# Kernel tuning notes

Hardware: AMD Instinct MI355X
Metric: run time of the kernel (lower is better)

## Reference

```python
import jax, jax.numpy as jnp
import numpy as np

EMB = 1024
HEAD = 64


def setup_inputs() -> dict:
    key = jax.random.key(0)
    kx, kq, kk, kv = jax.random.split(key, 4)
    x = jax.random.normal(kx, (4, 4096, EMB), dtype=jnp.float32)
    # nn.Linear(emb, head, bias=False): y = x @ W^T; store transposed [emb, head]
    s = 1.0 / np.sqrt(EMB)
    Wq = jax.random.uniform(kq, (EMB, HEAD), jnp.float32, -s, s)
    Wk = jax.random.uniform(kk, (EMB, HEAD), jnp.float32, -s, s)
    Wv = jax.random.uniform(kv, (EMB, HEAD), jnp.float32, -s, s)
    return {"x": x, "Wq": Wq, "Wk": Wk, "Wv": Wv}


def reference(x, Wq, Wk, Wv):
    # x: [B, T, E]; projections -> [B, T, H]
    Q = jnp.einsum("bte,eh->bth", x, Wq)
    K = jnp.einsum("bte,eh->bth", x, Wk)
    V = jnp.einsum("bte,eh->bth", x, Wv)
    scale = 1.0 / np.sqrt(HEAD).astype(np.float32)
    scores = jnp.einsum("bqh,bkh->bqk", Q, K) * scale  # [B, T, T]
    attn = jax.nn.softmax(scores, axis=-1)
    out = jnp.einsum("bqk,bkh->bqh", attn, V)  # [B, T, H]
    return out
```

## Files before the change

### kernel.cpp

```cpp
#include <hip/hip_runtime.h>
#include <hip/hip_bf16.h>

typedef __bf16 bf16x8 __attribute__((ext_vector_type(8)));
typedef float floatx4 __attribute__((ext_vector_type(4)));

#define B_ 4
#define T_ 4096
#define E_ 1024
#define H_ 64
#define NSEG 8
#define SEGLEN (T_ / NSEG)
#define NROWS (B_ * T_)

#define QSCALE 0.18033688011112042f

#if __has_builtin(__builtin_amdgcn_exp2f)
#define EXP2(x) __builtin_amdgcn_exp2f(x)
#else
#define EXP2(x) exp2f(x)
#endif

__device__ __forceinline__ floatx4 mfma16(bf16x8 a, bf16x8 b, floatx4 c) {
  return __builtin_amdgcn_mfma_f32_16x16x32_bf16(a, b, c, 0, 0, 0);
}

#define GLDS16(gp, lp)                                                        \
  __builtin_amdgcn_global_load_lds(                                           \
      (const __attribute__((address_space(1))) void*)(gp),                    \
      (__attribute__((address_space(3))) void*)(lp), 16, 0, 0)

__global__ void prep_wt_k(const float* __restrict__ Wq, const float* __restrict__ Wk,
                          const float* __restrict__ Wv, __bf16* __restrict__ Wfrag) {
  int gid = blockIdx.x * 4 + (threadIdx.x >> 6);
  int lane = threadIdx.x & 63;
  int ch = gid / 24, rem = gid % 24;
  int nt = rem >> 1, half = rem & 1;
  int g = lane >> 4, lm = lane & 15;
  int w = nt >> 2;
  const float* W = (w == 0) ? Wq : (w == 1) ? Wk : Wv;
  float sc = (w == 0) ? QSCALE : 1.0f;
  int h = (nt & 3) * 16 + lm;
  int e0 = ch * 64 + half * 32 + g * 8;
  __bf16* dst = Wfrag + (size_t)gid * 1024 / 2 + lane * 8;
  bf16x8 v;
#pragma unroll
  for (int j = 0; j < 8; j++) v[j] = (__bf16)(W[(size_t)(e0 + j) * H_ + h] * sc);
  *(bf16x8*)dst = v;
}

__global__ void proj_k(const float* __restrict__ x, const __bf16* __restrict__ Wfrag,
                       __bf16* __restrict__ Qo, __bf16* __restrict__ Ko,
                       __bf16* __restrict__ Vt) {
  __shared__ __align__(16) char sX[2 * 4096];

  int tid = threadIdx.x;
  int wv = tid >> 6, lane = tid & 63;
  int lm = lane & 15, g = lane >> 4;
  int row_base = blockIdx.x * 16;

  floatx4 acc[3];
#pragma unroll
  for (int i = 0; i < 3; i++) acc[i] = (floatx4)0.0f;

  const char* xb = (const char*)x;
  const char* wfb = (const char*)Wfrag;
  int srow = tid >> 4, sc = tid & 15;

#define PROJ_STAGE(buf, ec)                                                   \
  GLDS16(xb + (size_t)(row_base + srow) * 4096 + (size_t)(ec) * 4 +           \
             ((sc ^ srow) << 4),                                              \
         sX + (buf) * 4096 + tid * 16);

  PROJ_STAGE(0, 0);
  __syncthreads();

  for (int ch = 0; ch < 16; ch++) {
    if (ch + 1 < 16) PROJ_STAGE((ch + 1) & 1, (ch + 1) * 64);
    const char* xB = sX + (ch & 1) * 4096;

    bf16x8 b0[3], b1[3];
#pragma unroll
    for (int i = 0; i < 3; i++) {
      int nt = wv * 3 + i;
      const char* wp = wfb + ((size_t)(ch * 12 + nt) * 2) * 1024 + lane * 16;
      b0[i] = *(const bf16x8*)(wp);
      b1[i] = *(const bf16x8*)(wp + 1024);
    }
    const char* xp = xB + lm * 256;
    bf16x8 a[2];
#pragma unroll
    for (int ks = 0; ks < 2; ks++) {
      int c0 = ks * 8 + g * 2;
      float4 f0 = *(const float4*)(xp + ((c0 ^ lm) << 4));
      float4 f1 = *(const float4*)(xp + (((c0 + 1) ^ lm) << 4));
      a[ks][0] = (__bf16)f0.x; a[ks][1] = (__bf16)f0.y;
      a[ks][2] = (__bf16)f0.z; a[ks][3] = (__bf16)f0.w;
      a[ks][4] = (__bf16)f1.x; a[ks][5] = (__bf16)f1.y;
      a[ks][6] = (__bf16)f1.z; a[ks][7] = (__bf16)f1.w;
    }
#pragma unroll
    for (int i = 0; i < 3; i++) {
      acc[i] = mfma16(a[0], b0[i], acc[i]);
      acc[i] = mfma16(a[1], b1[i], acc[i]);
    }
    __syncthreads();
  }

#pragma unroll
  for (int i = 0; i < 3; i++) {
    int nt = wv * 3 + i;
    int w = nt >> 2;
    int h = (nt & 3) * 16 + lm;
#pragma unroll
    for (int r = 0; r < 4; r++) {
      __bf16 v = (__bf16)acc[i][r];
      int rr = row_base + g * 4 + r;
      if (w == 0)      Qo[(size_t)rr * H_ + h] = v;
      else if (w == 1) Ko[(size_t)rr * H_ + h] = v;
      else {
        int b = rr >> 12, t = rr & (T_ - 1);
        int kin = t & 63;
        int pos = ((kin >> 5) << 5) + (((kin >> 2) & 3) << 3) +
                  (((kin >> 4) & 1) << 2) + (kin & 3);
        Vt[((size_t)b * H_ + h) * T_ + (t & ~63) + pos] = v;
      }
    }
  }
}

__global__ __launch_bounds__(256, 2) void attn_k(
    const __bf16* __restrict__ Q, const __bf16* __restrict__ K,
    const __bf16* __restrict__ Vt, __bf16* __restrict__ Op, float* __restrict__ lp) {
  __shared__ __align__(16) char sK[2 * 8192];
  __shared__ __align__(16) char sV[2 * 8192];

  int qb = blockIdx.x, b = blockIdx.y, seg = blockIdx.z;
  int tid = threadIdx.x, wv = tid >> 6, lane = tid & 63;
  int lm = lane & 15, g = lane >> 4;
  int q0 = qb * 256 + wv * 64;

  const __bf16* Qb = Q + (size_t)b * T_ * H_;
  const char* Kb = (const char*)(K + (size_t)b * T_ * H_);
  const char* Vb = (const char*)(Vt + (size_t)b * H_ * T_);

  bf16x8 qf[4][2];
#pragma unroll
  for (int qi = 0; qi < 4; qi++)
#pragma unroll
    for (int hs = 0; hs < 2; hs++)
      qf[qi][hs] =
          *(const bf16x8*)&Qb[(size_t)(q0 + qi * 16 + lm) * H_ + hs * 32 + g * 8];

  floatx4 o_acc[4][4], o_l[4];
#pragma unroll
  for (int qi = 0; qi < 4; qi++) {
#pragma unroll
    for (int i = 0; i < 4; i++) o_acc[qi][i] = (floatx4)0.0f;
    o_l[qi] = (floatx4)0.0f;
  }

  bf16x8 vone;
#pragma unroll
  for (int j = 0; j < 8; j++) vone[j] = (__bf16)1.0f;

  int s3 = lm & 7;
  int koff[4][2], voff[2][4];
#pragma unroll
  for (int mt = 0; mt < 4; mt++) {
    koff[mt][0] = (mt * 16 + lm) * 128 + ((g ^ s3) << 4);
    koff[mt][1] = (mt * 16 + lm) * 128 + (((g + 4) ^ s3) << 4);
  }
#pragma unroll
  for (int ks = 0; ks < 2; ks++)
#pragma unroll
    for (int nt = 0; nt < 4; nt++)
      voff[ks][nt] = (nt * 16 + lm) * 128 + (((ks * 4 + g) ^ s3) << 4);

  int srow = tid >> 3, schk = tid & 7;
  int swz0 = (schk ^ (srow & 7)) << 4;

#define ATTN_STAGE(buf, k0_)                                                  \
  {                                                                           \
    int off = (buf) * 8192 + tid * 16;                                        \
    GLDS16(Kb + (size_t)(k0_ + srow) * 128 + swz0, sK + off);                 \
    GLDS16(Kb + (size_t)(k0_ + srow + 32) * 128 + swz0, sK + off + 4096);     \
    GLDS16(Vb + (size_t)srow * (T_ * 2) + (size_t)(k0_) * 2 + swz0, sV + off);\
    GLDS16(Vb + (size_t)(srow + 32) * (T_ * 2) + (size_t)(k0_) * 2 + swz0,    \
           sV + off + 4096);                                                  \
  }

  int kbase = seg * SEGLEN;
  ATTN_STAGE(0, kbase);
  __syncthreads();

  for (int t = 0; t < SEGLEN / 64; t++) {
    if (t + 1 < SEGLEN / 64) ATTN_STAGE((t + 1) & 1, kbase + (t + 1) * 64);
    const char* kB = sK + (t & 1) * 8192;
    const char* vB = sV + (t & 1) * 8192;

    floatx4 s_acc[4][4];
#pragma unroll
    for (int mt = 0; mt < 4; mt++)
#pragma unroll
      for (int qi = 0; qi < 4; qi++) s_acc[mt][qi] = (floatx4)0.0f;
#pragma unroll
    for (int mt = 0; mt < 4; mt++) {
      bf16x8 a0 = *(const bf16x8*)(kB + koff[mt][0]);
      bf16x8 a1 = *(const bf16x8*)(kB + koff[mt][1]);
#pragma unroll
      for (int qi = 0; qi < 4; qi++) {
        s_acc[mt][qi] = mfma16(a0, qf[qi][0], s_acc[mt][qi]);
        s_acc[mt][qi] = mfma16(a1, qf[qi][1], s_acc[mt][qi]);
      }
    }

    bf16x8 pa[4][2];
#pragma unroll
    for (int qi = 0; qi < 4; qi++)
#pragma unroll
      for (int mt = 0; mt < 4; mt++)
#pragma unroll
        for (int r = 0; r < 4; r++)
          pa[qi][mt >> 1][(mt & 1) * 4 + r] = (__bf16)EXP2(s_acc[mt][qi][r]);

#pragma unroll
    for (int ks = 0; ks < 2; ks++) {
      bf16x8 bb[4];
#pragma unroll
      for (int nt = 0; nt < 4; nt++) bb[nt] = *(const bf16x8*)(vB + voff[ks][nt]);
#pragma unroll
      for (int qi = 0; qi < 4; qi++) {
#pragma unroll
        for (int nt = 0; nt < 4; nt++)
          o_acc[qi][nt] = mfma16(pa[qi][ks], bb[nt], o_acc[qi][nt]);
        o_l[qi] = mfma16(pa[qi][ks], vone, o_l[qi]);
      }
    }
    __syncthreads();
  }

  size_t rowbase = (size_t)seg * NROWS + (size_t)b * T_ + qb * 256 + wv * 64;
#pragma unroll
  for (int qi = 0; qi < 4; qi++) {
#pragma unroll
    for (int nt = 0; nt < 4; nt++)
#pragma unroll
      for (int r = 0; r < 4; r++)
        Op[(rowbase + qi * 16 + g * 4 + r) * 64 + nt * 16 + lm] =
            (__bf16)o_acc[qi][nt][r];
    if (lm == 0) {
#pragma unroll
      for (int r = 0; r < 4; r++)
        lp[rowbase + qi * 16 + g * 4 + r] = o_l[qi][r];
    }
  }
}

__global__ void combine_k(const __bf16* __restrict__ Op, const float* __restrict__ lp,
                          float* __restrict__ out) {
  int idx = blockIdx.x * 256 + threadIdx.x;
  int row = idx >> 6;
  float L = 0.0f, o = 0.0f;
#pragma unroll
  for (int s = 0; s < NSEG; s++) {
    L += lp[(size_t)s * NROWS + row];
    o += (float)Op[(size_t)s * NROWS * 64 + idx];
  }
  out[idx] = o / L;
}

extern "C" void kernel_launch(void* const* d_in, const int* in_sizes, int n_in,
                              void* d_out, int out_size, void* d_ws, size_t ws_size,
                              hipStream_t stream) {
  const float* x  = (const float*)d_in[0];
  const float* Wq = (const float*)d_in[1];
  const float* Wk = (const float*)d_in[2];
  const float* Wv = (const float*)d_in[3];
  float* out = (float*)d_out;

  char* ws = (char*)d_ws;
  __bf16* Wf  = (__bf16*)(ws);
  __bf16* Qs  = (__bf16*)(ws + 0x60000);
  __bf16* Ks  = (__bf16*)(ws + 0x260000);
  __bf16* Vts = (__bf16*)(ws + 0x460000);
  __bf16* Op  = (__bf16*)(ws + 0x660000);
  float*  lp  = (float*)(ws + 0x1660000);

  prep_wt_k<<<96, 256, 0, stream>>>(Wq, Wk, Wv, Wf);
  proj_k<<<NROWS / 16, 256, 0, stream>>>(x, Wf, Qs, Ks, Vts);
  attn_k<<<dim3(T_ / 256, B_, NSEG), 256, 0, stream>>>(Qs, Ks, Vts, Op, lp);
  combine_k<<<NROWS * 64 / 256, 256, 0, stream>>>(Op, lp, out);
}
```

Measured before the change: 62.81 us.

## Load x directly into registers in projection, drop LDS staging and barriers

The projection kernel no longer stages x tiles through shared memory with async global-to-LDS copies and per-chunk barriers. Each wave now reads its own x row fragments straight from global memory into registers, prefetching the next chunk while the current one is used. Work is repartitioned so each block handles 32 rows, with each wave covering 16 rows and 6 of the 12 output column tiles instead of 3. The aim is to remove LDS traffic and synchronisation, at the cost of more registers and x rows being read twice from global memory (once per wave pair), relying on cache.

```diff
diff --git a/kernel.cpp b/kernel.cpp
--- a/kernel.cpp
+++ b/kernel.cpp
@@ -48,67 +48,60 @@
   *(bf16x8*)dst = v;
 }
 
-__global__ void proj_k(const float* __restrict__ x, const __bf16* __restrict__ Wfrag,
-                       __bf16* __restrict__ Qo, __bf16* __restrict__ Ko,
-                       __bf16* __restrict__ Vt) {
-  __shared__ __align__(16) char sX[2 * 4096];
-
+__global__ __launch_bounds__(256) void proj_k(
+    const float* __restrict__ x, const __bf16* __restrict__ Wfrag,
+    __bf16* __restrict__ Qo, __bf16* __restrict__ Ko, __bf16* __restrict__ Vt) {
   int tid = threadIdx.x;
   int wv = tid >> 6, lane = tid & 63;
   int lm = lane & 15, g = lane >> 4;
-  int row_base = blockIdx.x * 16;
-
-  floatx4 acc[3];
-#pragma unroll
-  for (int i = 0; i < 3; i++) acc[i] = (floatx4)0.0f;
-
-  const char* xb = (const char*)x;
-  const char* wfb = (const char*)Wfrag;
-  int srow = tid >> 4, sc = tid & 15;
-
-#define PROJ_STAGE(buf, ec)                                                   \
-  GLDS16(xb + (size_t)(row_base + srow) * 4096 + (size_t)(ec) * 4 +           \
-             ((sc ^ srow) << 4),                                              \
-         sX + (buf) * 4096 + tid * 16);
-
-  PROJ_STAGE(0, 0);
-  __syncthreads();
+  int rowjob = blockIdx.x * 2 + (wv >> 1);
+  int nth = wv & 1;
+  int row_base = rowjob * 16;
+
+  const float* xr = x + (size_t)(row_base + lm) * E_;
+  const char* wfb = (const char*)Wfrag + (size_t)(nth * 6 * 2) * 1024 + lane * 16;
+
+  floatx4 acc[6];
+#pragma unroll
+  for (int i = 0; i < 6; i++) acc[i] = (floatx4)0.0f;
+
+  float4 f[2][2];
+#pragma unroll
+  for (int ks = 0; ks < 2; ks++) {
+    f[ks][0] = *(const float4*)(xr + ks * 32 + g * 8);
+    f[ks][1] = *(const float4*)(xr + ks * 32 + g * 8 + 4);
+  }
 
   for (int ch = 0; ch < 16; ch++) {
-    if (ch + 1 < 16) PROJ_STAGE((ch + 1) & 1, (ch + 1) * 64);
-    const char* xB = sX + (ch & 1) * 4096;
-
-    bf16x8 b0[3], b1[3];
-#pragma unroll
-    for (int i = 0; i < 3; i++) {
-      int nt = wv * 3 + i;
-      const char* wp = wfb + ((size_t)(ch * 12 + nt) * 2) * 1024 + lane * 16;
-      b0[i] = *(const bf16x8*)(wp);
-      b1[i] = *(const bf16x8*)(wp + 1024);
-    }
-    const char* xp = xB + lm * 256;
     bf16x8 a[2];
 #pragma unroll
     for (int ks = 0; ks < 2; ks++) {
-      int c0 = ks * 8 + g * 2;
-      float4 f0 = *(const float4*)(xp + ((c0 ^ lm) << 4));
-      float4 f1 = *(const float4*)(xp + (((c0 + 1) ^ lm) << 4));
-      a[ks][0] = (__bf16)f0.x; a[ks][1] = (__bf16)f0.y;
-      a[ks][2] = (__bf16)f0.z; a[ks][3] = (__bf16)f0.w;
-      a[ks][4] = (__bf16)f1.x; a[ks][5] = (__bf16)f1.y;
-      a[ks][6] = (__bf16)f1.z; a[ks][7] = (__bf16)f1.w;
-    }
-#pragma unroll
-    for (int i = 0; i < 3; i++) {
-      acc[i] = mfma16(a[0], b0[i], acc[i]);
-      acc[i] = mfma16(a[1], b1[i], acc[i]);
-    }
-    __syncthreads();
-  }
-
-#pragma unroll
-  for (int i = 0; i < 3; i++) {
-    int nt = wv * 3 + i;
+      a[ks][0] = (__bf16)f[ks][0].x; a[ks][1] = (__bf16)f[ks][0].y;
+      a[ks][2] = (__bf16)f[ks][0].z; a[ks][3] = (__bf16)f[ks][0].w;
+      a[ks][4] = (__bf16)f[ks][1].x; a[ks][5] = (__bf16)f[ks][1].y;
+      a[ks][6] = (__bf16)f[ks][1].z; a[ks][7] = (__bf16)f[ks][1].w;
+    }
+    if (ch + 1 < 16) {
+      const float* xn = xr + (ch + 1) * 64 + g * 8;
+#pragma unroll
+      for (int ks = 0; ks < 2; ks++) {
+        f[ks][0] = *(const float4*)(xn + ks * 32);
+        f[ks][1] = *(const float4*)(xn + ks * 32 + 4);
+      }
+    }
+    const char* wp = wfb + (size_t)(ch * 24) * 1024;
+#pragma unroll
+    for (int i = 0; i < 6; i++) {
+      bf16x8 b0 = *(const bf16x8*)(wp + (size_t)(i * 2) * 1024);
+      bf16x8 b1 = *(const bf16x8*)(wp + (size_t)(i * 2 + 1) * 1024);
+      acc[i] = mfma16(a[0], b0, acc[i]);
+      acc[i] = mfma16(a[1], b1, acc[i]);
+    }
+  }
+
+#pragma unroll
+  for (int i = 0; i < 6; i++) {
+    int nt = nth * 6 + i;
     int w = nt >> 2;
     int h = (nt & 3) * 16 + lm;
 #pragma unroll
@@ -287,7 +280,7 @@
   float*  lp  = (float*)(ws + 0x1660000);
 
   prep_wt_k<<<96, 256, 0, stream>>>(Wq, Wk, Wv, Wf);
-  proj_k<<<NROWS / 16, 256, 0, stream>>>(x, Wf, Qs, Ks, Vts);
+  proj_k<<<NROWS / 32, 256, 0, stream>>>(x, Wf, Qs, Ks, Vts);
   attn_k<<<dim3(T_ / 256, B_, NSEG), 256, 0, stream>>>(Qs, Ks, Vts, Op, lp);
   combine_k<<<NROWS * 64 / 256, 256, 0, stream>>>(Op, lp, out);
 }
```

New measurement: 73.97 us. 17.8% more time.
